# Optimization experiments

Measured on AMD Instinct MI355X. Metric: run time of the kernel, lower is better.

The kernel has to match this reference:

```python
import jax, jax.numpy as jnp
import numpy as np

B, H, W, C = 64, 32, 32, 256
HZ, WZ = 16, 16
N = 64          # hidden_dim = n_proposals
K = 3           # dynamic depthwise kernel size
EPS = 1e-5


def _layernorm(x, g, b):
    mu = jnp.mean(x, axis=-1, keepdims=True)
    var = jnp.var(x, axis=-1, keepdims=True)
    return (x - mu) * jax.lax.rsqrt(var + EPS) * g + b


def setup_inputs() -> dict:
    key = jax.random.key(0)
    ks = jax.random.split(key, 8)
    s = 0.02  # weight init scale
    return {
        "x_feat": jax.random.normal(ks[0], (B, H, W, C), jnp.float32),
        "z_feat": jax.random.normal(ks[1], (B, HZ, WZ, C), jnp.float32),
        "Wz": jax.random.normal(ks[2], (C, N), jnp.float32) * s,
        "bz": jnp.zeros((N,), jnp.float32),
        "Wx": jax.random.normal(ks[3], (C, N), jnp.float32) * s,
        "bx": jnp.zeros((N,), jnp.float32),
        "Wdyn": jax.random.normal(ks[4], (C, N + K), jnp.float32) * s,
        "bdyn": jnp.zeros((N + K,), jnp.float32),
        "g_norm": jnp.ones((C,), jnp.float32),
        "b_norm": jnp.zeros((C,), jnp.float32),
        "Wp": jax.random.normal(ks[5], (C, 1), jnp.float32) * s,
        "bp": jnp.zeros((1,), jnp.float32),
        "g_ln": jnp.ones((C,), jnp.float32),
        "b_ln": jnp.zeros((C,), jnp.float32),
    }


def _dysep_conv_atten(query, value, Wdyn, bdyn, g_norm, b_norm):
    # query, value: [B, N, C]
    dy = query @ Wdyn + bdyn                      # [B, N, N+K]
    w_depth = dy[:, :, :K]                        # [B, N, K] per-channel depthwise kernels
    w_point = dy[:, :, K:]                        # [B, N, N] per-sample pointwise (1x1) weights
    # depthwise conv along C with 'same' padding (torch conv1d = cross-correlation)
    vpad = jnp.pad(value, ((0, 0), (0, 0), (1, 1)))
    depth = (w_depth[..., 0:1] * vpad[:, :, 0:C]
             + w_depth[..., 1:2] * vpad[:, :, 1:C + 1]
             + w_depth[..., 2:3] * vpad[:, :, 2:C + 2])
    depth = jax.nn.relu(depth)                    # [B, N, C]
    point = jnp.einsum('bnm,bmc->bnc', w_point, depth)
    return _layernorm(point, g_norm, b_norm)


def reference(x_feat, z_feat, Wz, bz, Wx, bx, Wdyn, bdyn,
              g_norm, b_norm, Wp, bp, g_ln, b_ln):
    # kernels from template features (detached in the original: kernels.detach())
    z_core = z_feat @ Wz + bz                                   # [B,HZ,WZ,N]
    kernels = jnp.einsum('bhwn,bhwc->bnc', z_core, z_feat)      # [B,N,C]
    kernels = jax.lax.stop_gradient(kernels)

    x_n = x_feat @ Wx + bx                                      # [B,H,W,N]
    kernels_x = jnp.einsum('bhwn,bhwc->bnc', x_n, x_feat)       # [B,N,C]
    kernels_x = _dysep_conv_atten(kernels, kernels_x, Wdyn, bdyn, g_norm, b_norm)

    x_corr = jnp.einsum('bnc,bhwn->bhwc', kernels_x, x_n)       # [B,H,W,C]
    proto = kernels_x @ Wp + bp                                 # [B,N,1]
    tem = jax.nn.sigmoid(jnp.einsum('bnd,bnc->bdc', proto, kernels_x))  # [B,1,C]
    tem = tem[:, :, None, :]                                    # [B,1,1,C]
    x_corr = x_corr * tem

    return x_feat + jax.nn.relu(_layernorm(x_corr, g_ln, b_ln))
```

## Files before the change

kernel.cpp:

```cpp
#include <hip/hip_runtime.h>
#include <math.h>

#define EPSV 1e-5f

typedef __attribute__((ext_vector_type(8))) short short8;
typedef __attribute__((ext_vector_type(4))) float f32x4;

static __device__ __forceinline__ unsigned bfpack2(float lo, float hi) {
    union { float f; unsigned u; } a, b;
    a.f = lo; b.f = hi;
    unsigned ua = a.u + 0x7fffu + ((a.u >> 16) & 1u);
    unsigned ub = b.u + 0x7fffu + ((b.u >> 16) & 1u);
    return (ua >> 16) | (ub & 0xffff0000u);
}
static __device__ __forceinline__ unsigned short bf1(float v) {
    return (unsigned short)bfpack2(v, 0.f);
}

__global__ __launch_bounds__(512) void gram(
    const float* __restrict__ Xx, const float* __restrict__ Xz,
    unsigned short* __restrict__ Gx, unsigned short* __restrict__ Gz,
    float* __restrict__ csx, float* __restrict__ csz)
{
    __shared__ __align__(16) unsigned short AT[128 * 72];
    __shared__ __align__(16) unsigned short BT[128 * 72];
    __shared__ float csr[16 * 128];
    const int id = blockIdx.x;
    const int b = id & 63;
    const int path = (id >> 6) & 1;
    const int tile = id >> 7;
    const bool diag = (tile < 2);
    const int ci = diag ? tile : 0;
    const float* X = path ? Xz : Xx;
    unsigned short* G = (path ? Gz : Gx) + (long)b * 65536;
    float* cs = path ? csz : csx;
    const int P = path ? 256 : 1024;
    const int nk = P >> 6;
    const int t = threadIdx.x;
    const int cq = (t & 31) * 4;
    const int ph = t >> 5;
    const int w = t >> 6;
    const int quad = (t >> 4) & 3, lane16 = t & 15;
    const float* Xb = X + (long)b * P * 256;
    const int colA = ci * 128;

    f32x4 acc[4][4] = {};
    float csA[4] = {0.f, 0.f, 0.f, 0.f};

    for (int kc = 0; kc < nk; ++kc) {
        const int p0 = kc * 64 + ph * 4;
        float4 va[4], vb[4];
#pragma unroll
        for (int k = 0; k < 4; ++k)
            va[k] = *(const float4*)(Xb + (long)(p0 + k) * 256 + colA + cq);
        if (!diag) {
#pragma unroll
            for (int k = 0; k < 4; ++k)
                vb[k] = *(const float4*)(Xb + (long)(p0 + k) * 256 + 128 + cq);
        }
        __syncthreads();
#pragma unroll
        for (int j = 0; j < 4; ++j) {
            const int row = cq + j;
            const int key = (row >> 2) & 7;
            uint2 pk;
            pk.x = bfpack2(((const float*)&va[0])[j], ((const float*)&va[1])[j]);
            pk.y = bfpack2(((const float*)&va[2])[j], ((const float*)&va[3])[j]);
            *(uint2*)&AT[row * 72 + (((ph >> 1) ^ key) << 3) + ((ph & 1) << 2)] = pk;
            if (diag)
                csA[j] += ((const float*)&va[0])[j] + ((const float*)&va[1])[j]
                        + ((const float*)&va[2])[j] + ((const float*)&va[3])[j];
        }
        if (!diag) {
#pragma unroll
            for (int j = 0; j < 4; ++j) {
                const int row = cq + j;
                const int key = (row >> 2) & 7;
                uint2 pk;
                pk.x = bfpack2(((const float*)&vb[0])[j], ((const float*)&vb[1])[j]);
                pk.y = bfpack2(((const float*)&vb[2])[j], ((const float*)&vb[3])[j]);
                *(uint2*)&BT[row * 72 + (((ph >> 1) ^ key) << 3) + ((ph & 1) << 2)] = pk;
            }
        }
        __syncthreads();
        if (diag) {
            const int wr = w >> 2, wc4 = w & 3;
#pragma unroll
            for (int ks = 0; ks < 2; ++ks) {
                const int slot = ks * 4 + quad;
                short8 bfr[2];
#pragma unroll
                for (int ni = 0; ni < 2; ++ni) {
                    const int rw = wc4 * 32 + ni * 16 + lane16;
                    bfr[ni] = *(const short8*)&AT[rw * 72 + ((slot ^ ((rw >> 2) & 7)) << 3)];
                }
#pragma unroll
                for (int mi = 0; mi < 4; ++mi) {
                    const int ra = wr * 64 + mi * 16 + lane16;
                    short8 afr = *(const short8*)&AT[ra * 72 + ((slot ^ ((ra >> 2) & 7)) << 3)];
#pragma unroll
                    for (int ni = 0; ni < 2; ++ni)
                        acc[mi][ni] = __builtin_amdgcn_mfma_f32_16x16x32_bf16(afr, bfr[ni], acc[mi][ni], 0, 0, 0);
                }
            }
        } else {
            const int sel = w >> 2, w2 = w & 3, wr = w2 >> 1, wc = w2 & 1;
            const unsigned short* As = sel ? BT : AT;
            const unsigned short* Bs = sel ? AT : BT;
#pragma unroll
            for (int ks = 0; ks < 2; ++ks) {
                const int slot = ks * 4 + quad;
                short8 bfr[4];
#pragma unroll
                for (int ni = 0; ni < 4; ++ni) {
                    const int rw = wc * 64 + ni * 16 + lane16;
                    bfr[ni] = *(const short8*)&Bs[rw * 72 + ((slot ^ ((rw >> 2) & 7)) << 3)];
                }
#pragma unroll
                for (int mi = 0; mi < 4; ++mi) {
                    const int ra = wr * 64 + mi * 16 + lane16;
                    short8 afr = *(const short8*)&As[ra * 72 + ((slot ^ ((ra >> 2) & 7)) << 3)];
#pragma unroll
                    for (int ni = 0; ni < 4; ++ni)
                        acc[mi][ni] = __builtin_amdgcn_mfma_f32_16x16x32_bf16(afr, bfr[ni], acc[mi][ni], 0, 0, 0);
                }
            }
        }
    }
    if (diag) {
        const int wr = w >> 2, wc4 = w & 3;
#pragma unroll
        for (int mi = 0; mi < 4; ++mi) {
            const int rbase = ci * 128 + wr * 64 + mi * 16 + quad * 4;
#pragma unroll
            for (int ni = 0; ni < 2; ++ni) {
                const int col = ci * 128 + wc4 * 32 + ni * 16 + lane16;
#pragma unroll
                for (int r = 0; r < 4; ++r)
                    G[(rbase + r) * 256 + col] = bf1(acc[mi][ni][r]);
            }
        }
#pragma unroll
        for (int j = 0; j < 4; ++j) csr[ph * 128 + cq + j] = csA[j];
        __syncthreads();
        if (t < 128) {
            float s = 0.f;
#pragma unroll
            for (int k = 0; k < 16; ++k) s += csr[k * 128 + t];
            cs[b * 256 + ci * 128 + t] = s;
        }
    } else {
        const int sel = w >> 2, w2 = w & 3, wr = w2 >> 1, wc = w2 & 1;
        const int R = sel ? 128 : 0, C = sel ? 0 : 128;
#pragma unroll
        for (int mi = 0; mi < 4; ++mi) {
            const int rbase = R + wr * 64 + mi * 16 + quad * 4;
#pragma unroll
            for (int ni = 0; ni < 4; ++ni) {
                const int col = C + wc * 64 + ni * 16 + lane16;
#pragma unroll
                for (int r = 0; r < 4; ++r)
                    G[(rbase + r) * 256 + col] = bf1(acc[mi][ni][r]);
            }
        }
    }
}

__global__ __launch_bounds__(256) void proj(
    const unsigned short* __restrict__ Gx, const float* __restrict__ csx,
    const float* __restrict__ Wx, const float* __restrict__ bx,
    float* __restrict__ kxr,
    const unsigned short* __restrict__ Gz, const float* __restrict__ csz,
    const float* __restrict__ Wz, const float* __restrict__ bz,
    const float* __restrict__ Wdyn, float* __restrict__ dypart)
{
    __shared__ __align__(16) unsigned short ATW[64 * 264];
    __shared__ float SLICE[64 * 68];
    __shared__ float WC2[64 * 68];
    __shared__ float WD3L[192];
    const int t = threadIdx.x;
    const int id = blockIdx.x;
    const int b = id & 63, s = id >> 6;
    const bool xp = (s < 4);
    const int ct = s & 3;
    const unsigned short* G = xp ? Gx : Gz;
    const float* cs   = xp ? csx : csz;
    const float* W    = xp ? Wx : Wz;
    const float* bias = xp ? bx : bz;
    const int n = t & 63, ph2 = t >> 6;
#pragma unroll
    for (int cc = 0; cc < 4; ++cc) {
        float v[16];
#pragma unroll
        for (int k = 0; k < 16; ++k) v[k] = W[(ph2 * 64 + cc * 16 + k) * 64 + n];
        uint4 p0, p1;
        p0.x = bfpack2(v[0], v[1]);   p0.y = bfpack2(v[2], v[3]);
        p0.z = bfpack2(v[4], v[5]);   p0.w = bfpack2(v[6], v[7]);
        p1.x = bfpack2(v[8], v[9]);   p1.y = bfpack2(v[10], v[11]);
        p1.z = bfpack2(v[12], v[13]); p1.w = bfpack2(v[14], v[15]);
        *(uint4*)&ATW[n * 264 + ph2 * 64 + cc * 16]     = p0;
        *(uint4*)&ATW[n * 264 + ph2 * 64 + cc * 16 + 8] = p1;
    }
    __syncthreads();
    const int w = t >> 6, quad = (t >> 4) & 3, lane16 = t & 15;
    const unsigned short* Grow =
        G + (long)(b * 256 + ct * 64 + w * 16 + lane16) * 256 + quad * 8;
    short8 bfr[8];
#pragma unroll
    for (int u = 0; u < 8; ++u) bfr[u] = *(const short8*)(Grow + u * 32);
    f32x4 acc[4] = {{0.f,0.f,0.f,0.f},{0.f,0.f,0.f,0.f},{0.f,0.f,0.f,0.f},{0.f,0.f,0.f,0.f}};
#pragma unroll
    for (int kc = 0; kc < 4; ++kc)
#pragma unroll
        for (int ks = 0; ks < 2; ++ks) {
            const int ko = ks * 32 + quad * 8;
            const short8 bfrag = bfr[kc * 2 + ks];
#pragma unroll
            for (int mi = 0; mi < 4; ++mi) {
                short8 afrag = *(const short8*)&ATW[(mi * 16 + lane16) * 264 + kc * 64 + ko];
                acc[mi] = __builtin_amdgcn_mfma_f32_16x16x32_bf16(afrag, bfrag, acc[mi], 0, 0, 0);
            }
        }
    const int col = ct * 64 + w * 16 + lane16;
    const float csv = cs[b * 256 + col];
    if (xp) {
#pragma unroll
        for (int mi = 0; mi < 4; ++mi) {
            const int nrow = mi * 16 + quad * 4;
#pragma unroll
            for (int r = 0; r < 4; ++r)
                kxr[((long)(b * 64 + nrow + r)) * 256 + col] = acc[mi][r] + bias[nrow + r] * csv;
        }
    } else {
        const int cloc = w * 16 + lane16;
#pragma unroll
        for (int mi = 0; mi < 4; ++mi) {
            const int nrow = mi * 16 + quad * 4;
#pragma unroll
            for (int r = 0; r < 4; ++r)
                SLICE[cloc * 68 + nrow + r] = acc[mi][r] + bias[nrow + r] * csv;
        }
        {
            const int m = t & 63, clg = t >> 6;
#pragma unroll
            for (int j = 0; j < 16; ++j) {
                const int cl = clg * 16 + j;
                WC2[cl * 68 + m] = Wdyn[((long)(ct * 64 + cl)) * 67 + 3 + m];
            }
            if (t < 192) WD3L[t] = Wdyn[((long)(ct * 64 + t / 3)) * 67 + (t % 3)];
        }
        __syncthreads();
        const int tr = t >> 4, tc = t & 15;
        float adv[4][4] = {};
#pragma unroll 16
        for (int cl = 0; cl < 64; ++cl) {
            float4 a  = *(float4*)&SLICE[cl * 68 + tr * 4];
            float4 wv = *(float4*)&WC2[cl * 68 + tc * 4];
            adv[0][0]+=a.x*wv.x; adv[0][1]+=a.x*wv.y; adv[0][2]+=a.x*wv.z; adv[0][3]+=a.x*wv.w;
            adv[1][0]+=a.y*wv.x; adv[1][1]+=a.y*wv.y; adv[1][2]+=a.y*wv.z; adv[1][3]+=a.y*wv.w;
            adv[2][0]+=a.z*wv.x; adv[2][1]+=a.z*wv.y; adv[2][2]+=a.z*wv.z; adv[2][3]+=a.z*wv.w;
            adv[3][0]+=a.w*wv.x; adv[3][1]+=a.w*wv.y; adv[3][2]+=a.w*wv.z; adv[3][3]+=a.w*wv.w;
        }
        const long base = (long)(b * 4 + ct) * 64;
#pragma unroll
        for (int i = 0; i < 4; ++i) {
            float4 o = make_float4(adv[i][0], adv[i][1], adv[i][2], adv[i][3]);
            *(float4*)(dypart + (base + tr * 4 + i) * 68 + tc * 4) = o;
        }
        if (t < 192) {
            const int nwd3 = t / 3, jwd3 = t - nwd3 * 3;
            float wdacc = 0.f;
#pragma unroll 16
            for (int cl = 0; cl < 64; ++cl)
                wdacc += SLICE[cl * 68 + nwd3] * WD3L[cl * 3 + jwd3];
            dypart[(base + nwd3) * 68 + 64 + jwd3] = wdacc;
        }
    }
}

__global__ __launch_bounds__(256) void depthpoint(
    const float* __restrict__ dyp, const float* __restrict__ bdyn,
    const float* __restrict__ v,
    const float* __restrict__ g, const float* __restrict__ Wp,
    float* __restrict__ point, float* __restrict__ partials)
{
    __shared__ float smem[13312];
    float* wpT = smem;
    float* wd3 = smem + 4352;
    float* vt  = smem + 4608;
    float* dep = smem + 8960;
    float* rs  = vt;

    const int t = threadIdx.x;
    const int b = blockIdx.y, ct = blockIdx.x, c0 = ct * 64;
    const int tr = t >> 4, tc = t & 15;

#pragma unroll
    for (int i = 0; i < 4; ++i) {
        int idx = t + i * 256; int n = idx >> 4, m0 = (idx & 15) * 4;
        float4 a0 = *(const float4*)(dyp + ((long)((b * 4 + 0) * 64 + n)) * 68 + m0);
        float4 a1 = *(const float4*)(dyp + ((long)((b * 4 + 1) * 64 + n)) * 68 + m0);
        float4 a2 = *(const float4*)(dyp + ((long)((b * 4 + 2) * 64 + n)) * 68 + m0);
        float4 a3 = *(const float4*)(dyp + ((long)((b * 4 + 3) * 64 + n)) * 68 + m0);
        float4 w4;
        w4.x = a0.x + a1.x + a2.x + a3.x + bdyn[3 + m0 + 0];
        w4.y = a0.y + a1.y + a2.y + a3.y + bdyn[3 + m0 + 1];
        w4.z = a0.z + a1.z + a2.z + a3.z + bdyn[3 + m0 + 2];
        w4.w = a0.w + a1.w + a2.w + a3.w + bdyn[3 + m0 + 3];
        wpT[(m0+0)*68 + n] = w4.x; wpT[(m0+1)*68 + n] = w4.y;
        wpT[(m0+2)*68 + n] = w4.z; wpT[(m0+3)*68 + n] = w4.w;
    }
    if (t < 64) {
        long o0 = ((long)((b * 4 + 0) * 64 + t)) * 68 + 64;
        long o1 = ((long)((b * 4 + 1) * 64 + t)) * 68 + 64;
        long o2 = ((long)((b * 4 + 2) * 64 + t)) * 68 + 64;
        long o3 = ((long)((b * 4 + 3) * 64 + t)) * 68 + 64;
#pragma unroll
        for (int j = 0; j < 3; ++j)
            wd3[t*4+j] = dyp[o0+j] + dyp[o1+j] + dyp[o2+j] + dyp[o3+j] + bdyn[j];
    }
    {
        int m = t >> 2, lc0 = (t & 3) * 17;
#pragma unroll
        for (int k = 0; k < 17; ++k) {
            int lc = lc0 + k;
            if (lc < 66) {
                int c = c0 - 1 + lc;
                vt[m * 68 + lc] = (c >= 0 && c < 256) ? v[((long)(b * 64 + m)) * 256 + c] : 0.f;
            }
        }
    }
    __syncthreads();
#pragma unroll
    for (int im = 0; im < 4; ++im) {
        int m = tr * 4 + im;
        float w0 = wd3[m*4+0], w1 = wd3[m*4+1], w2 = wd3[m*4+2];
#pragma unroll
        for (int jc = 0; jc < 4; ++jc) {
            int cl = tc * 4 + jc;
            float d = w0 * vt[m*68 + cl] + w1 * vt[m*68 + cl + 1] + w2 * vt[m*68 + cl + 2];
            dep[m*68 + cl] = fmaxf(d, 0.f);
        }
    }
    __syncthreads();
    float acc[4][4] = {};
#pragma unroll 16
    for (int m = 0; m < 64; ++m) {
        float4 a4 = *(float4*)&wpT[m * 68 + tr * 4];
        float4 d4 = *(float4*)&dep[m * 68 + tc * 4];
        acc[0][0]+=a4.x*d4.x; acc[0][1]+=a4.x*d4.y; acc[0][2]+=a4.x*d4.z; acc[0][3]+=a4.x*d4.w;
        acc[1][0]+=a4.y*d4.x; acc[1][1]+=a4.y*d4.y; acc[1][2]+=a4.y*d4.z; acc[1][3]+=a4.y*d4.w;
        acc[2][0]+=a4.z*d4.x; acc[2][1]+=a4.z*d4.y; acc[2][2]+=a4.z*d4.z; acc[2][3]+=a4.z*d4.w;
        acc[3][0]+=a4.w*d4.x; acc[3][1]+=a4.w*d4.y; acc[3][2]+=a4.w*d4.z; acc[3][3]+=a4.w*d4.w;
    }
    int cg = c0 + tc * 4;
    float4 g4  = *(const float4*)(g + cg);
    float4 wp4 = *(const float4*)(Wp + cg);
    float gw0 = g4.x*wp4.x, gw1 = g4.y*wp4.y, gw2 = g4.z*wp4.z, gw3 = g4.w*wp4.w;
#pragma unroll
    for (int i = 0; i < 4; ++i) {
        float4 o = make_float4(acc[i][0], acc[i][1], acc[i][2], acc[i][3]);
        *(float4*)(point + ((long)(b * 64 + tr * 4 + i)) * 256 + cg) = o;
        float s  = o.x + o.y + o.z + o.w;
        float s2 = o.x*o.x + o.y*o.y + o.z*o.z + o.w*o.w;
        float dg = o.x*gw0 + o.y*gw1 + o.z*gw2 + o.w*gw3;
        rs[0*1088 + (tr*4+i)*17 + tc] = s;
        rs[1*1088 + (tr*4+i)*17 + tc] = s2;
        rs[2*1088 + (tr*4+i)*17 + tc] = dg;
    }
    __syncthreads();
    if (t < 64) {
        float s = 0.f, s2 = 0.f, dg = 0.f;
#pragma unroll
        for (int j = 0; j < 16; ++j) {
            s  += rs[t*17 + j];
            s2 += rs[1088 + t*17 + j];
            dg += rs[2176 + t*17 + j];
        }
        long base = ((long)(b * 4 + ct)) * 192;
        partials[base + t]        = s;
        partials[base + 64 + t]   = s2;
        partials[base + 128 + t]  = dg;
    }
}

__global__ __launch_bounds__(256) void lntem(
    const float* __restrict__ partials, const float* __restrict__ point,
    const float* __restrict__ g, const float* __restrict__ bta,
    const float* __restrict__ Wp, const float* __restrict__ bp,
    float* __restrict__ murr, float* __restrict__ AB)
{
    __shared__ float sA[256], sB[256];
    __shared__ float wnv[64];
    __shared__ float tot[4];
    const int b = blockIdx.x, t = threadIdx.x;
    const int c = t;
    float gc = g[c], bc = bta[c], wpc = Wp[c];
    sA[t] = gc * wpc; sB[t] = bc * wpc;
    __syncthreads();
    for (int off = 128; off >= 1; off >>= 1) {
        if (t < off) { sA[t] += sA[t+off]; sB[t] += sB[t+off]; }
        __syncthreads();
    }
    if (t == 0) { tot[0] = sA[0]; tot[1] = sB[0] + bp[0]; }
    __syncthreads();
    float Sgw = tot[0], Sbw = tot[1];

    float protoe = 0.f, mu = 0.f, rr = 0.f;
    if (t < 64) {
        float S1 = 0.f, S2 = 0.f, Sdg = 0.f;
#pragma unroll
        for (int ct = 0; ct < 4; ++ct) {
            long o = ((long)(b * 4 + ct)) * 192;
            S1 += partials[o + t]; S2 += partials[o + 64 + t]; Sdg += partials[o + 128 + t];
        }
        mu = S1 * (1.f / 256.f);
        float var = S2 * (1.f / 256.f) - mu * mu;
        rr = rsqrtf(var + EPSV);
        protoe = rr * (Sdg - mu * Sgw) + Sbw;
        wnv[t] = protoe * rr;
        murr[b * 128 + 2*t]     = rr;
        murr[b * 128 + 2*t + 1] = -mu * rr;
    }
    __syncthreads();
    sA[t] = (t < 64) ? protoe * rr * mu : 0.f;
    sB[t] = (t < 64) ? protoe : 0.f;
    __syncthreads();
    for (int off = 128; off >= 1; off >>= 1) {
        if (t < off) { sA[t] += sA[t+off]; sB[t] += sB[t+off]; }
        __syncthreads();
    }
    if (t == 0) { tot[2] = sA[0]; tot[3] = sB[0]; }
    __syncthreads();
    float Bv = tot[2], Sv = tot[3];

    const float* pcol = point + (long)b * 64 * 256 + c;
    float a0 = 0.f, a1 = 0.f, a2 = 0.f, a3 = 0.f;
#pragma unroll
    for (int n = 0; n < 64; n += 4) {
        a0 += wnv[n+0] * pcol[(n+0) * 256];
        a1 += wnv[n+1] * pcol[(n+1) * 256];
        a2 += wnv[n+2] * pcol[(n+2) * 256];
        a3 += wnv[n+3] * pcol[(n+3) * 256];
    }
    float accA = a0 + a1 + a2 + a3;
    float x = gc * (accA - Bv) + bc * Sv;
    float temv = 1.f / (1.f + expf(-x));
    AB[b * 512 + c]       = gc * temv;
    AB[b * 512 + 256 + c] = bc * temv;
}

__global__ __launch_bounds__(256) void buildM(
    const float* __restrict__ point, const float* __restrict__ murr,
    const float* __restrict__ AB, const float* __restrict__ Wx,
    const float* __restrict__ bx,
    unsigned short* __restrict__ MT, float* __restrict__ svec)
{
    __shared__ float ks_s[64 * 68];
    __shared__ float wt_s[64 * 68];
    const int t = threadIdx.x;
    const int id = blockIdx.x;
    const int b = id & 63, mt = id >> 6;
    {
        const int n = t >> 2, q = t & 3;
        const float rn = murr[b * 128 + 2 * n], qn = murr[b * 128 + 2 * n + 1];
        const float* prow = point + ((long)(b * 64 + n)) * 256 + mt * 64 + q * 16;
        const float* Arow = AB + b * 512 + mt * 64 + q * 16;
#pragma unroll
        for (int j = 0; j < 4; ++j) {
            float4 p4 = *(const float4*)(prow + j * 4);
            float4 A4 = *(const float4*)(Arow + j * 4);
            float4 B4 = *(const float4*)(Arow + 256 + j * 4);
            float4 kv;
            kv.x = (p4.x * rn + qn) * A4.x + B4.x;
            kv.y = (p4.y * rn + qn) * A4.y + B4.y;
            kv.z = (p4.z * rn + qn) * A4.z + B4.z;
            kv.w = (p4.w * rn + qn) * A4.w + B4.w;
            *(float4*)&ks_s[n * 68 + q * 16 + j * 4] = kv;
        }
    }
    __syncthreads();
    if (t < 64) {
        float sv = 0.f;
#pragma unroll
        for (int n2 = 0; n2 < 64; ++n2) sv += bx[n2] * ks_s[n2 * 68 + t];
        svec[b * 256 + mt * 64 + t] = sv;
    }
    const int tr = t >> 4, tc = t & 15;
    const int nw = t & 63, ph = t >> 6;
    for (int cc = 0; cc < 4; ++cc) {
        float wv[16];
#pragma unroll
        for (int k = 0; k < 16; ++k) wv[k] = Wx[(cc * 64 + ph * 16 + k) * 64 + nw];
        __syncthreads();
#pragma unroll
        for (int k = 0; k < 16; ++k) wt_s[nw * 68 + ph * 16 + k] = wv[k];
        __syncthreads();
        float a2[4][4] = {};
#pragma unroll 16
        for (int n2 = 0; n2 < 64; ++n2) {
            float4 a4 = *(float4*)&ks_s[n2 * 68 + tr * 4];
            float4 w4 = *(float4*)&wt_s[n2 * 68 + tc * 4];
            a2[0][0]+=a4.x*w4.x; a2[0][1]+=a4.x*w4.y; a2[0][2]+=a4.x*w4.z; a2[0][3]+=a4.x*w4.w;
            a2[1][0]+=a4.y*w4.x; a2[1][1]+=a4.y*w4.y; a2[1][2]+=a4.y*w4.z; a2[1][3]+=a4.y*w4.w;
            a2[2][0]+=a4.z*w4.x; a2[2][1]+=a4.z*w4.y; a2[2][2]+=a4.z*w4.z; a2[2][3]+=a4.z*w4.w;
            a2[3][0]+=a4.w*w4.x; a2[3][1]+=a4.w*w4.y; a2[3][2]+=a4.w*w4.z; a2[3][3]+=a4.w*w4.w;
        }
#pragma unroll
        for (int i = 0; i < 4; ++i) {
            uint2 pk;
            pk.x = bfpack2(a2[i][0], a2[i][1]);
            pk.y = bfpack2(a2[i][2], a2[i][3]);
            *(uint2*)&MT[((long)(b * 256 + mt * 64 + tr * 4 + i)) * 256 + cc * 64 + tc * 4] = pk;
        }
    }
}

__global__ __launch_bounds__(256) void final2(
    const float* __restrict__ xf, const unsigned short* __restrict__ MT,
    const float* __restrict__ svec, const float* __restrict__ g,
    const float* __restrict__ bt, float* __restrict__ out)
{
    __shared__ __align__(16) float SlArr[32 * 132];
    __shared__ float red1[128], red2[128];
    __shared__ float muS[32], rrS[32];
    unsigned short* XT = (unsigned short*)SlArr;
    float* Sl = SlArr;
    const int t = threadIdx.x;
    const int id = blockIdx.x;
    const int b = id & 63, pt = id >> 6;
    const int w = t >> 6, quad = (t >> 4) & 3, lane16 = t & 15;
    const float* Xb = xf + ((long)(b * 1024 + pt * 32)) * 256;
    {
        const int p = t >> 3, q = t & 7;
#pragma unroll
        for (int i = 0; i < 8; ++i) {
            const int c = q * 32 + i * 4;
            float4 v = *(const float4*)(Xb + (long)p * 256 + c);
            uint2 pk;
            pk.x = bfpack2(v.x, v.y);
            pk.y = bfpack2(v.z, v.w);
            *(uint2*)&XT[p * 264 + c] = pk;
        }
    }
    __syncthreads();
    f32x4 acc[2][4] = {};
    const unsigned short* Mb = MT + (long)b * 65536 + quad * 8;
    short8 bf4[4];
#pragma unroll
    for (int ni = 0; ni < 4; ++ni)
        bf4[ni] = *(const short8*)(Mb + (long)(w * 64 + ni * 16 + lane16) * 256);
    for (int ks = 0; ks < 8; ++ks) {
        const int ko = ks * 32 + quad * 8;
        short8 nbf[4];
        if (ks + 1 < 8) {
#pragma unroll
            for (int ni = 0; ni < 4; ++ni)
                nbf[ni] = *(const short8*)(Mb + (long)(w * 64 + ni * 16 + lane16) * 256 + (ks + 1) * 32);
        }
        short8 af2[2];
#pragma unroll
        for (int mi = 0; mi < 2; ++mi)
            af2[mi] = *(const short8*)&XT[(mi * 16 + lane16) * 264 + ko];
#pragma unroll
        for (int mi = 0; mi < 2; ++mi)
#pragma unroll
            for (int ni = 0; ni < 4; ++ni)
                acc[mi][ni] = __builtin_amdgcn_mfma_f32_16x16x32_bf16(af2[mi], bf4[ni], acc[mi][ni], 0, 0, 0);
#pragma unroll
        for (int ni = 0; ni < 4; ++ni) bf4[ni] = nbf[ni];
    }
    float sv4[4];
#pragma unroll
    for (int ni = 0; ni < 4; ++ni) sv4[ni] = svec[b * 256 + w * 64 + ni * 16 + lane16];
#pragma unroll
    for (int mi = 0; mi < 2; ++mi)
#pragma unroll
        for (int r = 0; r < 4; ++r) {
            float s1 = 0.f, s2 = 0.f;
#pragma unroll
            for (int ni = 0; ni < 4; ++ni) {
                float v2 = acc[mi][ni][r] + sv4[ni];
                acc[mi][ni][r] = v2;
                s1 += v2; s2 += v2 * v2;
            }
#pragma unroll
            for (int m = 1; m <= 8; m <<= 1) {
                s1 += __shfl_xor(s1, m);
                s2 += __shfl_xor(s2, m);
            }
            if (lane16 == 0) {
                red1[(mi * 16 + quad * 4 + r) * 4 + w] = s1;
                red2[(mi * 16 + quad * 4 + r) * 4 + w] = s2;
            }
        }
    __syncthreads();
    if (t < 32) {
        float sa = red1[t*4] + red1[t*4+1] + red1[t*4+2] + red1[t*4+3];
        float sb = red2[t*4] + red2[t*4+1] + red2[t*4+2] + red2[t*4+3];
        float m = sa * (1.f / 256.f);
        muS[t] = m;
        rrS[t] = rsqrtf(sb * (1.f / 256.f) - m * m + EPSV);
    }
#pragma unroll
    for (int h = 0; h < 2; ++h) {
        __syncthreads();
        if ((w >> 1) == h) {
            const int chalf = (w & 1) * 64;
#pragma unroll
            for (int mi = 0; mi < 2; ++mi)
#pragma unroll
                for (int ni = 0; ni < 4; ++ni)
#pragma unroll
                    for (int r = 0; r < 4; ++r)
                        Sl[(mi * 16 + quad * 4 + r) * 132 + chalf + ni * 16 + lane16] = acc[mi][ni][r];
        }
        __syncthreads();
        {
            const int p = t >> 3, q = t & 7;
            const float m = muS[p], rr = rrS[p];
            const long grow = ((long)(b * 1024 + pt * 32 + p)) * 256;
#pragma unroll
            for (int j = 0; j < 4; ++j) {
                const int cl = q * 16 + j * 4;
                const int c = h * 128 + cl;
                float4 a  = *(float4*)&Sl[p * 132 + cl];
                float4 g4 = *(const float4*)(g + c);
                float4 b4 = *(const float4*)(bt + c);
                float4 xv = *(const float4*)(xf + grow + c);
                float4 o;
                o.x = xv.x + fmaxf((a.x - m) * rr * g4.x + b4.x, 0.f);
                o.y = xv.y + fmaxf((a.y - m) * rr * g4.y + b4.y, 0.f);
                o.z = xv.z + fmaxf((a.z - m) * rr * g4.z + b4.z, 0.f);
                o.w = xv.w + fmaxf((a.w - m) * rr * g4.w + b4.w, 0.f);
                *(float4*)(out + grow + c) = o;
            }
        }
    }
}

extern "C" void kernel_launch(void* const* d_in, const int* in_sizes, int n_in,
                              void* d_out, int out_size, void* d_ws, size_t ws_size,
                              hipStream_t stream)
{
    (void)in_sizes; (void)n_in; (void)out_size; (void)ws_size;
    const float* x_feat = (const float*)d_in[0];
    const float* z_feat = (const float*)d_in[1];
    const float* Wz     = (const float*)d_in[2];
    const float* bz     = (const float*)d_in[3];
    const float* Wx     = (const float*)d_in[4];
    const float* bx     = (const float*)d_in[5];
    const float* Wdyn   = (const float*)d_in[6];
    const float* bdyn   = (const float*)d_in[7];
    const float* g_norm = (const float*)d_in[8];
    const float* b_norm = (const float*)d_in[9];
    const float* Wp     = (const float*)d_in[10];
    const float* bp     = (const float*)d_in[11];
    const float* g_ln   = (const float*)d_in[12];
    const float* b_ln   = (const float*)d_in[13];
    float* out = (float*)d_out;

    float* ws       = (float*)d_ws;
    float* kxr      = ws;
    float* point    = kxr + 1048576;
    float* dypart   = point + 1048576;
    float* partials = dypart + 1114112;
    float* murr     = partials + 49152;
    float* AB       = murr + 8192;
    float* csx      = AB + 32768;
    float* csz      = csx + 16384;
    float* svec     = csz + 16384;
    unsigned short* Gx = (unsigned short*)(svec + 16384);
    unsigned short* Gz = Gx + 4194304;
    unsigned short* MT = Gz + 4194304;

    gram<<<384, 512, 0, stream>>>(x_feat, z_feat, Gx, Gz, csx, csz);
    proj<<<512, 256, 0, stream>>>(Gx, csx, Wx, bx, kxr, Gz, csz, Wz, bz,
                                  Wdyn, dypart);
    depthpoint<<<dim3(4, 64), 256, 0, stream>>>(dypart, bdyn, kxr, g_norm, Wp,
                                                point, partials);
    lntem<<<64, 256, 0, stream>>>(partials, point, g_norm, b_norm, Wp, bp, murr, AB);
    buildM<<<256, 256, 0, stream>>>(point, murr, AB, Wx, bx, MT, svec);
    final2<<<2048, 256, 0, stream>>>(x_feat, MT, svec, g_ln, b_ln, out);
}
```

Before: 280.0 us.

## Prefetch gram loads, fuse x-projection into depthpoint, merge lntem into buildM, shrink final tile

The gram kernel now software-pipelines its global loads, fetching the next 64-row chunk into registers while MFMAs run on the current one. The x-path projection moves out of proj and into the depthwise/pointwise kernel, with halo columns computed by a scalar dot product, so the kxr intermediate buffer goes away. lntem is folded into buildM, with each block recomputing the per-batch LN/tem statistics, which removes one launch and the murr/AB round trip. The final kernel uses 16-row tiles with direct per-element stores instead of staging through shared memory, doubling the grid; this trades redundant recomputation and less coalesced stores for fewer launches and less memory traffic.

```diff
diff --git a/kernel.cpp b/kernel.cpp
--- a/kernel.cpp
+++ b/kernel.cpp
@@ -15,6 +15,9 @@
 }
 static __device__ __forceinline__ unsigned short bf1(float v) {
     return (unsigned short)bfpack2(v, 0.f);
+}
+static __device__ __forceinline__ float b2f(unsigned short u) {
+    union { unsigned u; float f; } x; x.u = ((unsigned)u) << 16; return x.f;
 }
 
 __global__ __launch_bounds__(512) void gram(
@@ -47,9 +50,9 @@
     f32x4 acc[4][4] = {};
     float csA[4] = {0.f, 0.f, 0.f, 0.f};
 
-    for (int kc = 0; kc < nk; ++kc) {
-        const int p0 = kc * 64 + ph * 4;
-        float4 va[4], vb[4];
+    float4 va[4], vb[4];
+    {
+        const int p0 = ph * 4;
 #pragma unroll
         for (int k = 0; k < 4; ++k)
             va[k] = *(const float4*)(Xb + (long)(p0 + k) * 256 + colA + cq);
@@ -58,6 +61,9 @@
             for (int k = 0; k < 4; ++k)
                 vb[k] = *(const float4*)(Xb + (long)(p0 + k) * 256 + 128 + cq);
         }
+    }
+
+    for (int kc = 0; kc < nk; ++kc) {
         __syncthreads();
 #pragma unroll
         for (int j = 0; j < 4; ++j) {
@@ -83,6 +89,18 @@
             }
         }
         __syncthreads();
+        float4 nva[4], nvb[4];
+        if (kc + 1 < nk) {
+            const int p0 = (kc + 1) * 64 + ph * 4;
+#pragma unroll
+            for (int k = 0; k < 4; ++k)
+                nva[k] = *(const float4*)(Xb + (long)(p0 + k) * 256 + colA + cq);
+            if (!diag) {
+#pragma unroll
+                for (int k = 0; k < 4; ++k)
+                    nvb[k] = *(const float4*)(Xb + (long)(p0 + k) * 256 + 128 + cq);
+            }
+        }
         if (diag) {
             const int wr = w >> 2, wc4 = w & 3;
 #pragma unroll
@@ -126,6 +144,8 @@
                 }
             }
         }
+#pragma unroll
+        for (int k = 0; k < 4; ++k) { va[k] = nva[k]; vb[k] = nvb[k]; }
     }
     if (diag) {
         const int wr = w >> 2, wc4 = w & 3;
@@ -166,10 +186,7 @@
     }
 }
 
-__global__ __launch_bounds__(256) void proj(
-    const unsigned short* __restrict__ Gx, const float* __restrict__ csx,
-    const float* __restrict__ Wx, const float* __restrict__ bx,
-    float* __restrict__ kxr,
+__global__ __launch_bounds__(256) void projz(
     const unsigned short* __restrict__ Gz, const float* __restrict__ csz,
     const float* __restrict__ Wz, const float* __restrict__ bz,
     const float* __restrict__ Wdyn, float* __restrict__ dypart)
@@ -180,19 +197,13 @@
     __shared__ float WD3L[192];
     const int t = threadIdx.x;
     const int id = blockIdx.x;
-    const int b = id & 63, s = id >> 6;
-    const bool xp = (s < 4);
-    const int ct = s & 3;
-    const unsigned short* G = xp ? Gx : Gz;
-    const float* cs   = xp ? csx : csz;
-    const float* W    = xp ? Wx : Wz;
-    const float* bias = xp ? bx : bz;
+    const int b = id & 63, ct = id >> 6;
     const int n = t & 63, ph2 = t >> 6;
 #pragma unroll
     for (int cc = 0; cc < 4; ++cc) {
         float v[16];
 #pragma unroll
-        for (int k = 0; k < 16; ++k) v[k] = W[(ph2 * 64 + cc * 16 + k) * 64 + n];
+        for (int k = 0; k < 16; ++k) v[k] = Wz[(ph2 * 64 + cc * 16 + k) * 64 + n];
         uint4 p0, p1;
         p0.x = bfpack2(v[0], v[1]);   p0.y = bfpack2(v[2], v[3]);
         p0.z = bfpack2(v[4], v[5]);   p0.w = bfpack2(v[6], v[7]);
@@ -204,7 +215,7 @@
     __syncthreads();
     const int w = t >> 6, quad = (t >> 4) & 3, lane16 = t & 15;
     const unsigned short* Grow =
-        G + (long)(b * 256 + ct * 64 + w * 16 + lane16) * 256 + quad * 8;
+        Gz + (long)(b * 256 + ct * 64 + w * 16 + lane16) * 256 + quad * 8;
     short8 bfr[8];
 #pragma unroll
     for (int u = 0; u < 8; ++u) bfr[u] = *(const short8*)(Grow + u * 32);
@@ -222,78 +233,71 @@
             }
         }
     const int col = ct * 64 + w * 16 + lane16;
-    const float csv = cs[b * 256 + col];
-    if (xp) {
-#pragma unroll
-        for (int mi = 0; mi < 4; ++mi) {
-            const int nrow = mi * 16 + quad * 4;
-#pragma unroll
-            for (int r = 0; r < 4; ++r)
-                kxr[((long)(b * 64 + nrow + r)) * 256 + col] = acc[mi][r] + bias[nrow + r] * csv;
-        }
-    } else {
-        const int cloc = w * 16 + lane16;
-#pragma unroll
-        for (int mi = 0; mi < 4; ++mi) {
-            const int nrow = mi * 16 + quad * 4;
-#pragma unroll
-            for (int r = 0; r < 4; ++r)
-                SLICE[cloc * 68 + nrow + r] = acc[mi][r] + bias[nrow + r] * csv;
-        }
-        {
-            const int m = t & 63, clg = t >> 6;
-#pragma unroll
-            for (int j = 0; j < 16; ++j) {
-                const int cl = clg * 16 + j;
-                WC2[cl * 68 + m] = Wdyn[((long)(ct * 64 + cl)) * 67 + 3 + m];
-            }
-            if (t < 192) WD3L[t] = Wdyn[((long)(ct * 64 + t / 3)) * 67 + (t % 3)];
-        }
-        __syncthreads();
-        const int tr = t >> 4, tc = t & 15;
-        float adv[4][4] = {};
+    const float csv = csz[b * 256 + col];
+    const int cloc = w * 16 + lane16;
+#pragma unroll
+    for (int mi = 0; mi < 4; ++mi) {
+        const int nrow = mi * 16 + quad * 4;
+#pragma unroll
+        for (int r = 0; r < 4; ++r)
+            SLICE[cloc * 68 + nrow + r] = acc[mi][r] + bz[nrow + r] * csv;
+    }
+    {
+        const int m = t & 63, clg = t >> 6;
+#pragma unroll
+        for (int j = 0; j < 16; ++j) {
+            const int cl = clg * 16 + j;
+            WC2[cl * 68 + m] = Wdyn[((long)(ct * 64 + cl)) * 67 + 3 + m];
+        }
+        if (t < 192) WD3L[t] = Wdyn[((long)(ct * 64 + t / 3)) * 67 + (t % 3)];
+    }
+    __syncthreads();
+    const int tr = t >> 4, tc = t & 15;
+    float adv[4][4] = {};
 #pragma unroll 16
-        for (int cl = 0; cl < 64; ++cl) {
-            float4 a  = *(float4*)&SLICE[cl * 68 + tr * 4];
-            float4 wv = *(float4*)&WC2[cl * 68 + tc * 4];
-            adv[0][0]+=a.x*wv.x; adv[0][1]+=a.x*wv.y; adv[0][2]+=a.x*wv.z; adv[0][3]+=a.x*wv.w;
-            adv[1][0]+=a.y*wv.x; adv[1][1]+=a.y*wv.y; adv[1][2]+=a.y*wv.z; adv[1][3]+=a.y*wv.w;
-            adv[2][0]+=a.z*wv.x; adv[2][1]+=a.z*wv.y; adv[2][2]+=a.z*wv.z; adv[2][3]+=a.z*wv.w;
-            adv[3][0]+=a.w*wv.x; adv[3][1]+=a.w*wv.y; adv[3][2]+=a.w*wv.z; adv[3][3]+=a.w*wv.w;
-        }
-        const long base = (long)(b * 4 + ct) * 64;
-#pragma unroll
-        for (int i = 0; i < 4; ++i) {
-            float4 o = make_float4(adv[i][0], adv[i][1], adv[i][2], adv[i][3]);
-            *(float4*)(dypart + (base + tr * 4 + i) * 68 + tc * 4) = o;
-        }
-        if (t < 192) {
-            const int nwd3 = t / 3, jwd3 = t - nwd3 * 3;
-            float wdacc = 0.f;
+    for (int cl = 0; cl < 64; ++cl) {
+        float4 a  = *(float4*)&SLICE[cl * 68 + tr * 4];
+        float4 wv = *(float4*)&WC2[cl * 68 + tc * 4];
+        adv[0][0]+=a.x*wv.x; adv[0][1]+=a.x*wv.y; adv[0][2]+=a.x*wv.z; adv[0][3]+=a.x*wv.w;
+        adv[1][0]+=a.y*wv.x; adv[1][1]+=a.y*wv.y; adv[1][2]+=a.y*wv.z; adv[1][3]+=a.y*wv.w;
+        adv[2][0]+=a.z*wv.x; adv[2][1]+=a.z*wv.y; adv[2][2]+=a.z*wv.z; adv[2][3]+=a.z*wv.w;
+        adv[3][0]+=a.w*wv.x; adv[3][1]+=a.w*wv.y; adv[3][2]+=a.w*wv.z; adv[3][3]+=a.w*wv.w;
+    }
+    const long base = (long)(b * 4 + ct) * 64;
+#pragma unroll
+    for (int i = 0; i < 4; ++i) {
+        float4 o = make_float4(adv[i][0], adv[i][1], adv[i][2], adv[i][3]);
+        *(float4*)(dypart + (base + tr * 4 + i) * 68 + tc * 4) = o;
+    }
+    if (t < 192) {
+        const int nwd3 = t / 3, jwd3 = t - nwd3 * 3;
+        float wdacc = 0.f;
 #pragma unroll 16
-            for (int cl = 0; cl < 64; ++cl)
-                wdacc += SLICE[cl * 68 + nwd3] * WD3L[cl * 3 + jwd3];
-            dypart[(base + nwd3) * 68 + 64 + jwd3] = wdacc;
-        }
-    }
-}
-
-__global__ __launch_bounds__(256) void depthpoint(
+        for (int cl = 0; cl < 64; ++cl)
+            wdacc += SLICE[cl * 68 + nwd3] * WD3L[cl * 3 + jwd3];
+        dypart[(base + nwd3) * 68 + 64 + jwd3] = wdacc;
+    }
+}
+
+__global__ __launch_bounds__(256) void dpx(
+    const unsigned short* __restrict__ Gx, const float* __restrict__ csx,
+    const float* __restrict__ Wx, const float* __restrict__ bx,
     const float* __restrict__ dyp, const float* __restrict__ bdyn,
-    const float* __restrict__ v,
     const float* __restrict__ g, const float* __restrict__ Wp,
     float* __restrict__ point, float* __restrict__ partials)
 {
-    __shared__ float smem[13312];
-    float* wpT = smem;
-    float* wd3 = smem + 4352;
-    float* vt  = smem + 4608;
-    float* dep = smem + 8960;
+    __shared__ __align__(16) unsigned char pool[53248];
+    unsigned short* ATW = (unsigned short*)pool;
+    float* vt  = (float*)pool;
+    float* dep = (float*)(pool + 17408);
+    float* wpT = (float*)(pool + 34816);
+    float* wd3 = (float*)(pool + 52224);
     float* rs  = vt;
 
     const int t = threadIdx.x;
     const int b = blockIdx.y, ct = blockIdx.x, c0 = ct * 64;
     const int tr = t >> 4, tc = t & 15;
+    const int w = t >> 6, quad = (t >> 4) & 3, lane16 = t & 15;
 
 #pragma unroll
     for (int i = 0; i < 4; ++i) {
@@ -320,15 +324,73 @@
             wd3[t*4+j] = dyp[o0+j] + dyp[o1+j] + dyp[o2+j] + dyp[o3+j] + bdyn[j];
     }
     {
-        int m = t >> 2, lc0 = (t & 3) * 17;
-#pragma unroll
-        for (int k = 0; k < 17; ++k) {
-            int lc = lc0 + k;
-            if (lc < 66) {
-                int c = c0 - 1 + lc;
-                vt[m * 68 + lc] = (c >= 0 && c < 256) ? v[((long)(b * 64 + m)) * 256 + c] : 0.f;
-            }
-        }
+        const int n = t & 63, ph2 = t >> 6;
+#pragma unroll
+        for (int cc = 0; cc < 4; ++cc) {
+            float v[16];
+#pragma unroll
+            for (int k = 0; k < 16; ++k) v[k] = Wx[(ph2 * 64 + cc * 16 + k) * 64 + n];
+            uint4 p0, p1;
+            p0.x = bfpack2(v[0], v[1]);   p0.y = bfpack2(v[2], v[3]);
+            p0.z = bfpack2(v[4], v[5]);   p0.w = bfpack2(v[6], v[7]);
+            p1.x = bfpack2(v[8], v[9]);   p1.y = bfpack2(v[10], v[11]);
+            p1.z = bfpack2(v[12], v[13]); p1.w = bfpack2(v[14], v[15]);
+            *(uint4*)&ATW[n * 264 + ph2 * 64 + cc * 16]     = p0;
+            *(uint4*)&ATW[n * 264 + ph2 * 64 + cc * 16 + 8] = p1;
+        }
+    }
+    __syncthreads();
+    const unsigned short* Grow =
+        Gx + (long)(b * 256 + c0 + w * 16 + lane16) * 256 + quad * 8;
+    short8 bfr[8];
+#pragma unroll
+    for (int u = 0; u < 8; ++u) bfr[u] = *(const short8*)(Grow + u * 32);
+    f32x4 pacc[4] = {{0.f,0.f,0.f,0.f},{0.f,0.f,0.f,0.f},{0.f,0.f,0.f,0.f},{0.f,0.f,0.f,0.f}};
+#pragma unroll
+    for (int kc = 0; kc < 4; ++kc)
+#pragma unroll
+        for (int ks = 0; ks < 2; ++ks) {
+            const int ko = ks * 32 + quad * 8;
+            const short8 bfrag = bfr[kc * 2 + ks];
+#pragma unroll
+            for (int mi = 0; mi < 4; ++mi) {
+                short8 afrag = *(const short8*)&ATW[(mi * 16 + lane16) * 264 + kc * 64 + ko];
+                pacc[mi] = __builtin_amdgcn_mfma_f32_16x16x32_bf16(afrag, bfrag, pacc[mi], 0, 0, 0);
+            }
+        }
+    float edgeval = 0.f;
+    if (t < 128) {
+        const int n = t & 63, e = t >> 6;
+        const int colg = e ? (c0 + 64) : (c0 - 1);
+        if (colg >= 0 && colg < 256) {
+            const unsigned short* gr = Gx + ((long)(b * 256 + colg)) * 256;
+            float accd = 0.f;
+#pragma unroll 8
+            for (int k = 0; k < 256; k += 8) {
+                short8 gs = *(const short8*)(gr + k);
+                short8 wsv = *(const short8*)&ATW[n * 264 + k];
+#pragma unroll
+                for (int j = 0; j < 8; ++j)
+                    accd += b2f((unsigned short)gs[j]) * b2f((unsigned short)wsv[j]);
+            }
+            edgeval = accd + bx[n] * csx[b * 256 + colg];
+        }
+    }
+    __syncthreads();
+    {
+        const float csv = csx[b * 256 + c0 + w * 16 + lane16];
+        const int lc = 1 + w * 16 + lane16;
+#pragma unroll
+        for (int mi = 0; mi < 4; ++mi) {
+            const int nrow = mi * 16 + quad * 4;
+#pragma unroll
+            for (int r = 0; r < 4; ++r)
+                vt[(nrow + r) * 68 + lc] = pacc[mi][r] + bx[nrow + r] * csv;
+        }
+    }
+    if (t < 128) {
+        const int n = t & 63, e = t >> 6;
+        vt[n * 68 + (e ? 65 : 0)] = edgeval;
     }
     __syncthreads();
 #pragma unroll
@@ -384,93 +446,87 @@
     }
 }
 
-__global__ __launch_bounds__(256) void lntem(
+__global__ __launch_bounds__(256) void lnbuild(
     const float* __restrict__ partials, const float* __restrict__ point,
     const float* __restrict__ g, const float* __restrict__ bta,
     const float* __restrict__ Wp, const float* __restrict__ bp,
-    float* __restrict__ murr, float* __restrict__ AB)
+    const float* __restrict__ Wx, const float* __restrict__ bx,
+    unsigned short* __restrict__ MT, float* __restrict__ svec)
 {
     __shared__ float sA[256], sB[256];
     __shared__ float wnv[64];
     __shared__ float tot[4];
-    const int b = blockIdx.x, t = threadIdx.x;
-    const int c = t;
-    float gc = g[c], bc = bta[c], wpc = Wp[c];
-    sA[t] = gc * wpc; sB[t] = bc * wpc;
-    __syncthreads();
-    for (int off = 128; off >= 1; off >>= 1) {
-        if (t < off) { sA[t] += sA[t+off]; sB[t] += sB[t+off]; }
-        __syncthreads();
-    }
-    if (t == 0) { tot[0] = sA[0]; tot[1] = sB[0] + bp[0]; }
-    __syncthreads();
-    float Sgw = tot[0], Sbw = tot[1];
-
-    float protoe = 0.f, mu = 0.f, rr = 0.f;
-    if (t < 64) {
-        float S1 = 0.f, S2 = 0.f, Sdg = 0.f;
-#pragma unroll
-        for (int ct = 0; ct < 4; ++ct) {
-            long o = ((long)(b * 4 + ct)) * 192;
-            S1 += partials[o + t]; S2 += partials[o + 64 + t]; Sdg += partials[o + 128 + t];
-        }
-        mu = S1 * (1.f / 256.f);
-        float var = S2 * (1.f / 256.f) - mu * mu;
-        rr = rsqrtf(var + EPSV);
-        protoe = rr * (Sdg - mu * Sgw) + Sbw;
-        wnv[t] = protoe * rr;
-        murr[b * 128 + 2*t]     = rr;
-        murr[b * 128 + 2*t + 1] = -mu * rr;
-    }
-    __syncthreads();
-    sA[t] = (t < 64) ? protoe * rr * mu : 0.f;
-    sB[t] = (t < 64) ? protoe : 0.f;
-    __syncthreads();
-    for (int off = 128; off >= 1; off >>= 1) {
-        if (t < off) { sA[t] += sA[t+off]; sB[t] += sB[t+off]; }
-        __syncthreads();
-    }
-    if (t == 0) { tot[2] = sA[0]; tot[3] = sB[0]; }
-    __syncthreads();
-    float Bv = tot[2], Sv = tot[3];
-
-    const float* pcol = point + (long)b * 64 * 256 + c;
-    float a0 = 0.f, a1 = 0.f, a2 = 0.f, a3 = 0.f;
-#pragma unroll
-    for (int n = 0; n < 64; n += 4) {
-        a0 += wnv[n+0] * pcol[(n+0) * 256];
-        a1 += wnv[n+1] * pcol[(n+1) * 256];
-        a2 += wnv[n+2] * pcol[(n+2) * 256];
-        a3 += wnv[n+3] * pcol[(n+3) * 256];
-    }
-    float accA = a0 + a1 + a2 + a3;
-    float x = gc * (accA - Bv) + bc * Sv;
-    float temv = 1.f / (1.f + expf(-x));
-    AB[b * 512 + c]       = gc * temv;
-    AB[b * 512 + 256 + c] = bc * temv;
-}
-
-__global__ __launch_bounds__(256) void buildM(
-    const float* __restrict__ point, const float* __restrict__ murr,
-    const float* __restrict__ AB, const float* __restrict__ Wx,
-    const float* __restrict__ bx,
-    unsigned short* __restrict__ MT, float* __restrict__ svec)
-{
+    __shared__ float MURR[128];
+    __shared__ float ABL[512];
     __shared__ float ks_s[64 * 68];
     __shared__ float wt_s[64 * 68];
-    const int t = threadIdx.x;
     const int id = blockIdx.x;
     const int b = id & 63, mt = id >> 6;
+    const int t = threadIdx.x;
+    {
+        const int c = t;
+        float gc = g[c], bc = bta[c], wpc = Wp[c];
+        sA[t] = gc * wpc; sB[t] = bc * wpc;
+        __syncthreads();
+        for (int off = 128; off >= 1; off >>= 1) {
+            if (t < off) { sA[t] += sA[t+off]; sB[t] += sB[t+off]; }
+            __syncthreads();
+        }
+        if (t == 0) { tot[0] = sA[0]; tot[1] = sB[0] + bp[0]; }
+        __syncthreads();
+        float Sgw = tot[0], Sbw = tot[1];
+
+        float protoe = 0.f, mu = 0.f, rr = 0.f;
+        if (t < 64) {
+            float S1 = 0.f, S2 = 0.f, Sdg = 0.f;
+#pragma unroll
+            for (int ct = 0; ct < 4; ++ct) {
+                long o = ((long)(b * 4 + ct)) * 192;
+                S1 += partials[o + t]; S2 += partials[o + 64 + t]; Sdg += partials[o + 128 + t];
+            }
+            mu = S1 * (1.f / 256.f);
+            float var = S2 * (1.f / 256.f) - mu * mu;
+            rr = rsqrtf(var + EPSV);
+            protoe = rr * (Sdg - mu * Sgw) + Sbw;
+            wnv[t] = protoe * rr;
+            MURR[2*t] = rr; MURR[2*t + 1] = -mu * rr;
+        }
+        __syncthreads();
+        sA[t] = (t < 64) ? protoe * rr * mu : 0.f;
+        sB[t] = (t < 64) ? protoe : 0.f;
+        __syncthreads();
+        for (int off = 128; off >= 1; off >>= 1) {
+            if (t < off) { sA[t] += sA[t+off]; sB[t] += sB[t+off]; }
+            __syncthreads();
+        }
+        if (t == 0) { tot[2] = sA[0]; tot[3] = sB[0]; }
+        __syncthreads();
+        float Bv = tot[2], Sv = tot[3];
+
+        const float* pcol = point + (long)b * 64 * 256 + c;
+        float a0 = 0.f, a1 = 0.f, a2 = 0.f, a3 = 0.f;
+#pragma unroll
+        for (int n = 0; n < 64; n += 4) {
+            a0 += wnv[n+0] * pcol[(n+0) * 256];
+            a1 += wnv[n+1] * pcol[(n+1) * 256];
+            a2 += wnv[n+2] * pcol[(n+2) * 256];
+            a3 += wnv[n+3] * pcol[(n+3) * 256];
+        }
+        float accA = a0 + a1 + a2 + a3;
+        float x = gc * (accA - Bv) + bc * Sv;
+        float temv = 1.f / (1.f + expf(-x));
+        ABL[c] = gc * temv; ABL[256 + c] = bc * temv;
+    }
+    __syncthreads();
     {
         const int n = t >> 2, q = t & 3;
-        const float rn = murr[b * 128 + 2 * n], qn = murr[b * 128 + 2 * n + 1];
+        const float rn = MURR[2 * n], qn = MURR[2 * n + 1];
         const float* prow = point + ((long)(b * 64 + n)) * 256 + mt * 64 + q * 16;
-        const float* Arow = AB + b * 512 + mt * 64 + q * 16;
 #pragma unroll
         for (int j = 0; j < 4; ++j) {
             float4 p4 = *(const float4*)(prow + j * 4);
-            float4 A4 = *(const float4*)(Arow + j * 4);
-            float4 B4 = *(const float4*)(Arow + 256 + j * 4);
+            float4 A4 = *(float4*)&ABL[mt * 64 + q * 16 + j * 4];
+            float4 B4 = *(float4*)&ABL[256 + mt * 64 + q * 16 + j * 4];
             float4 kv;
             kv.x = (p4.x * rn + qn) * A4.x + B4.x;
             kv.y = (p4.y * rn + qn) * A4.y + B4.y;
@@ -516,57 +572,52 @@
     }
 }
 
-__global__ __launch_bounds__(256) void final2(
+__global__ __launch_bounds__(256) void final3(
     const float* __restrict__ xf, const unsigned short* __restrict__ MT,
     const float* __restrict__ svec, const float* __restrict__ g,
     const float* __restrict__ bt, float* __restrict__ out)
 {
-    __shared__ __align__(16) float SlArr[32 * 132];
-    __shared__ float red1[128], red2[128];
-    __shared__ float muS[32], rrS[32];
-    unsigned short* XT = (unsigned short*)SlArr;
-    float* Sl = SlArr;
+    __shared__ __align__(16) unsigned short XT[16 * 264];
+    __shared__ float red1[64], red2[64];
     const int t = threadIdx.x;
     const int id = blockIdx.x;
     const int b = id & 63, pt = id >> 6;
     const int w = t >> 6, quad = (t >> 4) & 3, lane16 = t & 15;
-    const float* Xb = xf + ((long)(b * 1024 + pt * 32)) * 256;
     {
-        const int p = t >> 3, q = t & 7;
-#pragma unroll
-        for (int i = 0; i < 8; ++i) {
-            const int c = q * 32 + i * 4;
-            float4 v = *(const float4*)(Xb + (long)p * 256 + c);
-            uint2 pk;
-            pk.x = bfpack2(v.x, v.y);
-            pk.y = bfpack2(v.z, v.w);
-            *(uint2*)&XT[p * 264 + c] = pk;
-        }
-    }
-    __syncthreads();
-    f32x4 acc[2][4] = {};
+        const int p = t >> 4, q = t & 15;
+        const float* Xr = xf + ((long)(b * 1024 + pt * 16 + p)) * 256 + q * 16;
+        float4 v0 = *(const float4*)(Xr + 0);
+        float4 v1 = *(const float4*)(Xr + 4);
+        float4 v2 = *(const float4*)(Xr + 8);
+        float4 v3 = *(const float4*)(Xr + 12);
+        uint4 pk0;
+        pk0.x = bfpack2(v0.x, v0.y); pk0.y = bfpack2(v0.z, v0.w);
+        pk0.z = bfpack2(v1.x, v1.y); pk0.w = bfpack2(v1.z, v1.w);
+        uint4 pk1;
+        pk1.x = bfpack2(v2.x, v2.y); pk1.y = bfpack2(v2.z, v2.w);
+        pk1.z = bfpack2(v3.x, v3.y); pk1.w = bfpack2(v3.z, v3.w);
+        *(uint4*)&XT[p * 264 + q * 16]     = pk0;
+        *(uint4*)&XT[p * 264 + q * 16 + 8] = pk1;
+    }
+    __syncthreads();
+    f32x4 acc[4] = {{0.f,0.f,0.f,0.f},{0.f,0.f,0.f,0.f},{0.f,0.f,0.f,0.f},{0.f,0.f,0.f,0.f}};
     const unsigned short* Mb = MT + (long)b * 65536 + quad * 8;
     short8 bf4[4];
 #pragma unroll
     for (int ni = 0; ni < 4; ++ni)
         bf4[ni] = *(const short8*)(Mb + (long)(w * 64 + ni * 16 + lane16) * 256);
+#pragma unroll
     for (int ks = 0; ks < 8; ++ks) {
-        const int ko = ks * 32 + quad * 8;
         short8 nbf[4];
         if (ks + 1 < 8) {
 #pragma unroll
             for (int ni = 0; ni < 4; ++ni)
                 nbf[ni] = *(const short8*)(Mb + (long)(w * 64 + ni * 16 + lane16) * 256 + (ks + 1) * 32);
         }
-        short8 af2[2];
-#pragma unroll
-        for (int mi = 0; mi < 2; ++mi)
-            af2[mi] = *(const short8*)&XT[(mi * 16 + lane16) * 264 + ko];
-#pragma unroll
-        for (int mi = 0; mi < 2; ++mi)
-#pragma unroll
-            for (int ni = 0; ni < 4; ++ni)
-                acc[mi][ni] = __builtin_amdgcn_mfma_f32_16x16x32_bf16(af2[mi], bf4[ni], acc[mi][ni], 0, 0, 0);
+        short8 af = *(const short8*)&XT[lane16 * 264 + ks * 32 + quad * 8];
+#pragma unroll
+        for (int ni = 0; ni < 4; ++ni)
+            acc[ni] = __builtin_amdgcn_mfma_f32_16x16x32_bf16(af, bf4[ni], acc[ni], 0, 0, 0);
 #pragma unroll
         for (int ni = 0; ni < 4; ++ni) bf4[ni] = nbf[ni];
     }
@@ -574,67 +625,39 @@
 #pragma unroll
     for (int ni = 0; ni < 4; ++ni) sv4[ni] = svec[b * 256 + w * 64 + ni * 16 + lane16];
 #pragma unroll
-    for (int mi = 0; mi < 2; ++mi)
-#pragma unroll
-        for (int r = 0; r < 4; ++r) {
-            float s1 = 0.f, s2 = 0.f;
-#pragma unroll
-            for (int ni = 0; ni < 4; ++ni) {
-                float v2 = acc[mi][ni][r] + sv4[ni];
-                acc[mi][ni][r] = v2;
-                s1 += v2; s2 += v2 * v2;
-            }
-#pragma unroll
-            for (int m = 1; m <= 8; m <<= 1) {
-                s1 += __shfl_xor(s1, m);
-                s2 += __shfl_xor(s2, m);
-            }
-            if (lane16 == 0) {
-                red1[(mi * 16 + quad * 4 + r) * 4 + w] = s1;
-                red2[(mi * 16 + quad * 4 + r) * 4 + w] = s2;
-            }
-        }
-    __syncthreads();
-    if (t < 32) {
-        float sa = red1[t*4] + red1[t*4+1] + red1[t*4+2] + red1[t*4+3];
-        float sb = red2[t*4] + red2[t*4+1] + red2[t*4+2] + red2[t*4+3];
+    for (int r = 0; r < 4; ++r) {
+        float s1 = 0.f, s2 = 0.f;
+#pragma unroll
+        for (int ni = 0; ni < 4; ++ni) {
+            float v2 = acc[ni][r] + sv4[ni];
+            acc[ni][r] = v2;
+            s1 += v2; s2 += v2 * v2;
+        }
+#pragma unroll
+        for (int m = 1; m <= 8; m <<= 1) {
+            s1 += __shfl_xor(s1, m);
+            s2 += __shfl_xor(s2, m);
+        }
+        if (lane16 == 0) {
+            red1[(quad * 4 + r) * 4 + w] = s1;
+            red2[(quad * 4 + r) * 4 + w] = s2;
+        }
+    }
+    __syncthreads();
+#pragma unroll
+    for (int r = 0; r < 4; ++r) {
+        const int row = quad * 4 + r;
+        float sa = red1[row * 4] + red1[row * 4 + 1] + red1[row * 4 + 2] + red1[row * 4 + 3];
+        float sb = red2[row * 4] + red2[row * 4 + 1] + red2[row * 4 + 2] + red2[row * 4 + 3];
         float m = sa * (1.f / 256.f);
-        muS[t] = m;
-        rrS[t] = rsqrtf(sb * (1.f / 256.f) - m * m + EPSV);
-    }
-#pragma unroll
-    for (int h = 0; h < 2; ++h) {
-        __syncthreads();
-        if ((w >> 1) == h) {
-            const int chalf = (w & 1) * 64;
-#pragma unroll
-            for (int mi = 0; mi < 2; ++mi)
-#pragma unroll
-                for (int ni = 0; ni < 4; ++ni)
-#pragma unroll
-                    for (int r = 0; r < 4; ++r)
-                        Sl[(mi * 16 + quad * 4 + r) * 132 + chalf + ni * 16 + lane16] = acc[mi][ni][r];
-        }
-        __syncthreads();
-        {
-            const int p = t >> 3, q = t & 7;
-            const float m = muS[p], rr = rrS[p];
-            const long grow = ((long)(b * 1024 + pt * 32 + p)) * 256;
-#pragma unroll
-            for (int j = 0; j < 4; ++j) {
-                const int cl = q * 16 + j * 4;
-                const int c = h * 128 + cl;
-                float4 a  = *(float4*)&Sl[p * 132 + cl];
-                float4 g4 = *(const float4*)(g + c);
-                float4 b4 = *(const float4*)(bt + c);
-                float4 xv = *(const float4*)(xf + grow + c);
-                float4 o;
-                o.x = xv.x + fmaxf((a.x - m) * rr * g4.x + b4.x, 0.f);
-                o.y = xv.y + fmaxf((a.y - m) * rr * g4.y + b4.y, 0.f);
-                o.z = xv.z + fmaxf((a.z - m) * rr * g4.z + b4.z, 0.f);
-                o.w = xv.w + fmaxf((a.w - m) * rr * g4.w + b4.w, 0.f);
-                *(float4*)(out + grow + c) = o;
-            }
+        float rr = rsqrtf(sb * (1.f / 256.f) - m * m + EPSV);
+        const long grow = ((long)(b * 1024 + pt * 16 + row)) * 256;
+#pragma unroll
+        for (int ni = 0; ni < 4; ++ni) {
+            const int col = w * 64 + ni * 16 + lane16;
+            float a = acc[ni][r];
+            float o = xf[grow + col] + fmaxf((a - m) * rr * g[col] + bt[col], 0.f);
+            out[grow + col] = o;
         }
     }
 }
@@ -661,13 +684,10 @@
     float* out = (float*)d_out;
 
     float* ws       = (float*)d_ws;
-    float* kxr      = ws;
-    float* point    = kxr + 1048576;
+    float* point    = ws;
     float* dypart   = point + 1048576;
     float* partials = dypart + 1114112;
-    float* murr     = partials + 49152;
-    float* AB       = murr + 8192;
-    float* csx      = AB + 32768;
+    float* csx      = partials + 49152;
     float* csz      = csx + 16384;
     float* svec     = csz + 16384;
     unsigned short* Gx = (unsigned short*)(svec + 16384);
@@ -675,11 +695,10 @@
     unsigned short* MT = Gz + 4194304;
 
     gram<<<384, 512, 0, stream>>>(x_feat, z_feat, Gx, Gz, csx, csz);
-    proj<<<512, 256, 0, stream>>>(Gx, csx, Wx, bx, kxr, Gz, csz, Wz, bz,
-                                  Wdyn, dypart);
-    depthpoint<<<dim3(4, 64), 256, 0, stream>>>(dypart, bdyn, kxr, g_norm, Wp,
-                                                point, partials);
-    lntem<<<64, 256, 0, stream>>>(partials, point, g_norm, b_norm, Wp, bp, murr, AB);
-    buildM<<<256, 256, 0, stream>>>(point, murr, AB, Wx, bx, MT, svec);
-    final2<<<2048, 256, 0, stream>>>(x_feat, MT, svec, g_ln, b_ln, out);
-}
+    projz<<<256, 256, 0, stream>>>(Gz, csz, Wz, bz, Wdyn, dypart);
+    dpx<<<dim3(4, 64), 256, 0, stream>>>(Gx, csx, Wx, bx, dypart, bdyn,
+                                         g_norm, Wp, point, partials);
+    lnbuild<<<256, 256, 0, stream>>>(partials, point, g_norm, b_norm, Wp, bp,
+                                     Wx, bx, MT, svec);
+    final3<<<4096, 256, 0, stream>>>(x_feat, MT, svec, g_ln, b_ln, out);
+}
```

Result: no change. 285.0 us (+1.8%).
